# Optimization experiments

Hardware: AMD Instinct MI355X
Metric: run time of the kernel (lower is better)

The kernel has to match this reference:

```python
import jax, jax.numpy as jnp
import numpy as np

D = 2048      # feature dim (fc1 = Linear(2*2048, 2048))
S = 10240


def setup_inputs() -> dict:
    key = jax.random.key(0)
    ks = jax.random.split(key, 16)
    sc = 0.02
    z = lambda *s: jnp.zeros(s, jnp.float32)
    return {
        "x0": jax.random.normal(ks[0], (1, 1, D), jnp.float32),
        "x1": jax.random.normal(ks[1], (1, S, D), jnp.float32),
        # fc1: Linear(4096, 2048)  (stored input-major for x @ W)
        "W1": jax.random.normal(ks[2], (2 * D, D), jnp.float32) * sc,
        "b1": z(D),
        # fc2: Linear(2048, 1)
        "W2": jax.random.normal(ks[3], (D, 1), jnp.float32) * sc,
        "b2": z(1),
        # LSTM(input=1, hidden=1, bidirectional): per-direction gate params [4] = (i,f,g,o)
        "Wih_f": jax.random.normal(ks[4], (4,), jnp.float32) * 0.5,
        "Whh_f": jax.random.normal(ks[5], (4,), jnp.float32) * 0.5,
        "bih_f": z(4),
        "bhh_f": z(4),
        "Wih_b": jax.random.normal(ks[6], (4,), jnp.float32) * 0.5,
        "Whh_b": jax.random.normal(ks[7], (4,), jnp.float32) * 0.5,
        "bih_b": z(4),
        "bhh_b": z(4),
        # fc3: Linear(10, 1)
        "W3": jax.random.normal(ks[8], (10, 1), jnp.float32) * sc,
        "b3": z(1),
    }


def _lstm_dir(x_seq, Wih, Whh, bih, bhh):
    """Single-direction LSTM, input_size=hidden_size=1, batch=1.
    x_seq: [S] scalars. Returns h sequence [S]. PyTorch gate order (i,f,g,o)."""
    b = bih + bhh

    def step(carry, x):
        h, c = carry
        g = Wih * x + Whh * h + b              # [4]
        i = jax.nn.sigmoid(g[0])
        f = jax.nn.sigmoid(g[1])
        gg = jnp.tanh(g[2])
        o = jax.nn.sigmoid(g[3])
        c = f * c + i * gg
        h = o * jnp.tanh(c)
        return (h, c), h

    h0 = jnp.zeros((), x_seq.dtype)
    c0 = jnp.zeros((), x_seq.dtype)
    _, hs = jax.lax.scan(step, (h0, c0), x_seq)
    return hs


def reference(x0, x1, W1, b1, W2, b2,
              Wih_f, Whh_f, bih_f, bhh_f,
              Wih_b, Whh_b, bih_b, bhh_b,
              W3, b3):
    # similarity: cat(|x0 - x1|, x0 + x1) along features (x0 broadcasts over S)
    sim = jnp.concatenate([jnp.abs(x0 - x1), x0 + x1], axis=2)   # [1, S, 2D]
    h = jax.nn.relu(jnp.einsum('bsf,fd->bsd', sim, W1) + b1)     # [1, S, D]
    # (dropout is identity in eval mode)
    s = jax.nn.sigmoid(jnp.einsum('bsd,do->bso', h, W2) + b2)    # [1, S, 1]
    x_seq = s[0, :, 0]                                           # [S]

    h_f = _lstm_dir(x_seq, Wih_f, Whh_f, bih_f, bhh_f)           # [S]
    h_b = _lstm_dir(x_seq[::-1], Wih_b, Whh_b, bih_b, bhh_b)[::-1]
    out = jnp.stack([h_f, h_b], axis=1)                          # [S, 2] == lstm out [S,1,2]

    grp = out.reshape(1, -1, 10)                                 # [1, S*2/10, 10]
    y = jax.nn.sigmoid(grp @ W3 + b3)                            # [1, S*2/10, 1]
    return y.reshape(1, -1)
```

## Files before the change

kernel.cpp:

```cpp
#include <hip/hip_runtime.h>
#include <hip/hip_bf16.h>

#define DD 2048
#define SS 10240
#define KK 4096

typedef __bf16 bf16x8 __attribute__((ext_vector_type(8)));
typedef float  f32x4  __attribute__((ext_vector_type(4)));

__device__ __forceinline__ unsigned short f2bf_rne(float x) {
    unsigned int u = __float_as_uint(x);
    u += 0x7FFFu + ((u >> 16) & 1u);
    return (unsigned short)(u >> 16);
}

__global__ __launch_bounds__(256) void prep_kernel(
    const float* __restrict__ W1, const float* __restrict__ b2,
    unsigned short* __restrict__ W1T, float* __restrict__ s_pre) {
    __shared__ float tile[64][65];
    const int t = threadIdx.x;
    const int bf = blockIdx.x % (KK / 64);
    const int bd = blockIdx.x / (KK / 64);
    const int f0 = bf * 64, d0 = bd * 64;

#pragma unroll
    for (int p = 0; p < 4; ++p) {
        int fr = p * 16 + (t >> 4);
        int dc = (t & 15) * 4;
        const float4 v = *(const float4*)&W1[(size_t)(f0 + fr) * DD + d0 + dc];
        tile[fr][dc + 0] = v.x; tile[fr][dc + 1] = v.y;
        tile[fr][dc + 2] = v.z; tile[fr][dc + 3] = v.w;
    }
    __syncthreads();
#pragma unroll
    for (int p = 0; p < 4; ++p) {
        int dr = p * 16 + (t >> 4);
        int fc = (t & 15) * 4;
        ushort4 o;
        o.x = f2bf_rne(tile[fc + 0][dr]);
        o.y = f2bf_rne(tile[fc + 1][dr]);
        o.z = f2bf_rne(tile[fc + 2][dr]);
        o.w = f2bf_rne(tile[fc + 3][dr]);
        *(ushort4*)&W1T[(size_t)(d0 + dr) * KK + f0 + fc] = o;
    }
    int gid = blockIdx.x * 256 + t;
    if (gid < SS) s_pre[gid] = b2[0];
}

__global__ __launch_bounds__(256) void sim_kernel(
    const float* __restrict__ x0, const float* __restrict__ x1,
    unsigned short* __restrict__ simB) {
    const int s = blockIdx.x;
    const int d = threadIdx.x * 8;
    const float4 a0 = *(const float4*)&x0[d];
    const float4 a1 = *(const float4*)&x0[d + 4];
    const float4 v0 = *(const float4*)&x1[(size_t)s * DD + d];
    const float4 v1 = *(const float4*)&x1[(size_t)s * DD + d + 4];
    ushort4 lo0, lo1, hi0, hi1;
    lo0.x = f2bf_rne(fabsf(a0.x - v0.x)); hi0.x = f2bf_rne(a0.x + v0.x);
    lo0.y = f2bf_rne(fabsf(a0.y - v0.y)); hi0.y = f2bf_rne(a0.y + v0.y);
    lo0.z = f2bf_rne(fabsf(a0.z - v0.z)); hi0.z = f2bf_rne(a0.z + v0.z);
    lo0.w = f2bf_rne(fabsf(a0.w - v0.w)); hi0.w = f2bf_rne(a0.w + v0.w);
    lo1.x = f2bf_rne(fabsf(a1.x - v1.x)); hi1.x = f2bf_rne(a1.x + v1.x);
    lo1.y = f2bf_rne(fabsf(a1.y - v1.y)); hi1.y = f2bf_rne(a1.y + v1.y);
    lo1.z = f2bf_rne(fabsf(a1.z - v1.z)); hi1.z = f2bf_rne(a1.z + v1.z);
    lo1.w = f2bf_rne(fabsf(a1.w - v1.w)); hi1.w = f2bf_rne(a1.w + v1.w);
    unsigned short* row = &simB[(size_t)s * KK];
    *(ushort4*)&row[d]          = lo0;
    *(ushort4*)&row[d + 4]      = lo1;
    *(ushort4*)&row[DD + d]     = hi0;
    *(ushort4*)&row[DD + d + 4] = hi1;
}

#define BM3 320
#define BN3 256
#define BK3 64
#define NKT (KK / BK3)

#define STAGE_A(ktv, BUFV)                                                     \
    _Pragma("unroll")                                                          \
    for (int L = 0; L < 5; ++L) {                                              \
        __builtin_amdgcn_global_load_lds(                                      \
            (const __attribute__((address_space(1))) void*)(gA + (size_t)L * 64 * KK + (size_t)(ktv) * 64), \
            (__attribute__((address_space(3))) void*)&lds[BUFV][t * 8 + L * 4096], \
            16, 0, 0);                                                         \
    }
#define STAGE_B(ktv, BUFV)                                                     \
    _Pragma("unroll")                                                          \
    for (int L = 0; L < 4; ++L) {                                              \
        __builtin_amdgcn_global_load_lds(                                      \
            (const __attribute__((address_space(1))) void*)(gB + (size_t)L * 64 * KK + (size_t)(ktv) * 64), \
            (__attribute__((address_space(3))) void*)&lds[BUFV][20480 + t * 8 + L * 4096], \
            16, 0, 0);                                                         \
    }

#define BODY(ktv, BUF, SA_LIT, SB_LIT, DO_STAGE)                               \
    {                                                                          \
        asm volatile("s_waitcnt vmcnt(" SA_LIT ")" ::: "memory");              \
        __builtin_amdgcn_s_barrier();                                          \
        __builtin_amdgcn_sched_barrier(0);                                     \
        if (DO_STAGE) { STAGE_A((ktv) + 1, BUF ^ 1) }                          \
        asm volatile("s_waitcnt vmcnt(" SB_LIT ")" ::: "memory");              \
        __builtin_amdgcn_s_barrier();                                          \
        __builtin_amdgcn_sched_barrier(0);                                     \
        if (DO_STAGE) { STAGE_B((ktv) + 1, BUF ^ 1) }                          \
        _Pragma("unroll")                                                      \
        for (int ks = 0; ks < 2; ++ks) {                                       \
            const int gx = ks ? gx1 : gx0;                                     \
            _Pragma("unroll")                                                  \
            for (int h = 0; h < 2; ++h) {                                      \
                bf16x8 bfr[4];                                                 \
                _Pragma("unroll")                                              \
                for (int n = 0; n < 4; ++n)                                    \
                    bfr[n] = *(const bf16x8*)&lds[BUF][boff + (h * 4 + n) * 1024 + gx]; \
                _Pragma("unroll")                                              \
                for (int m = 0; m < 5; ++m) {                                  \
                    bf16x8 afr = *(const bf16x8*)&lds[BUF][aoff + m * 1024 + gx]; \
                    __builtin_amdgcn_s_setprio(1);                             \
                    _Pragma("unroll")                                          \
                    for (int n = 0; n < 4; ++n)                                \
                        acc[m][h * 4 + n] = __builtin_amdgcn_mfma_f32_16x16x32_bf16( \
                            afr, bfr[n], acc[m][h * 4 + n], 0, 0, 0);          \
                    __builtin_amdgcn_s_setprio(0);                             \
                }                                                              \
            }                                                                  \
        }                                                                      \
    }

__global__ __launch_bounds__(512, 2) void gemm3_kernel(
    const unsigned short* __restrict__ simB,
    const unsigned short* __restrict__ W1T,
    const float* __restrict__ b1, const float* __restrict__ W2,
    float* __restrict__ s_pre) {
    __shared__ unsigned short lds[2][36864];

    const int t    = threadIdx.x;
    const int lane = t & 63;
    const int wv   = t >> 6;
    const int wr   = wv >> 1;
    const int wc   = wv & 1;
    const int lr   = lane & 15;
    const int g4   = lane >> 4;
    const int l7   = lane & 7;

    const int bn = blockIdx.x & 7;
    const int bm = blockIdx.x >> 3;
    const int m0 = bm * BM3, n0 = bn * BN3;

    const int trow = t >> 3;
    const int gsrc = (t & 7) ^ (trow & 7);
    const unsigned short* gA = simB + (size_t)(m0 + trow) * KK + gsrc * 8;
    const unsigned short* gB = W1T  + (size_t)(n0 + trow) * KK + gsrc * 8;

    const int aoff = (wr * 80 + lr) * 64;
    const int boff = 20480 + (wc * 128 + lr) * 64;
    const int gx0  = ((0 * 4 + g4) ^ l7) * 8;
    const int gx1  = ((1 * 4 + g4) ^ l7) * 8;

    f32x4 acc[5][8];
#pragma unroll
    for (int m = 0; m < 5; ++m)
#pragma unroll
        for (int n = 0; n < 8; ++n)
            acc[m][n] = (f32x4){0.f, 0.f, 0.f, 0.f};

    STAGE_A(0, 0)
    STAGE_B(0, 0)

#pragma unroll 1
    for (int kt = 0; kt < NKT - 2; kt += 2) {
        BODY(kt,     0, "4", "5", 1)
        BODY(kt + 1, 1, "4", "5", 1)
    }
    BODY(NKT - 2, 0, "4", "5", 1)
    BODY(NKT - 1, 1, "4", "0", 0)

    float b1v[8], w2v[8];
#pragma unroll
    for (int n = 0; n < 8; ++n) {
        int col = n0 + wc * 128 + n * 16 + lr;
        b1v[n] = b1[col];
        w2v[n] = W2[col];
    }
#pragma unroll
    for (int m = 0; m < 5; ++m) {
#pragma unroll
        for (int r = 0; r < 4; ++r) {
            float rowsum = 0.f;
#pragma unroll
            for (int n = 0; n < 8; ++n) {
                float v = acc[m][n][r] + b1v[n];
                v = fmaxf(v, 0.f);
                rowsum = fmaf(v, w2v[n], rowsum);
            }
            rowsum += __shfl_xor(rowsum, 1);
            rowsum += __shfl_xor(rowsum, 2);
            rowsum += __shfl_xor(rowsum, 4);
            rowsum += __shfl_xor(rowsum, 8);
            if (lr == 0) {
                int row = m0 + wr * 80 + m * 16 + g4 * 4 + r;
                atomicAdd(&s_pre[row], rowsum);
            }
        }
    }
}

#define BM 128
#define BN 128
#define BK 32

__global__ __launch_bounds__(256) void gemm_kernel(
    const float* __restrict__ x0, const float* __restrict__ x1,
    const unsigned short* __restrict__ W1T,
    const float* __restrict__ b1, const float* __restrict__ W2,
    float* __restrict__ s_pre) {
    __shared__ unsigned short As[BM][BK];
    __shared__ unsigned short Bs[BN][BK];

    const int tid  = threadIdx.x;
    const int lane = tid & 63;
    const int wave = tid >> 6;
    const int wr = wave >> 1, wc = wave & 1;
    const int bm = blockIdx.x / (DD / BN);
    const int bn = blockIdx.x % (DD / BN);
    const int m0 = bm * BM, n0 = bn * BN;
    const int lr = lane & 15;
    const int lk = (lane >> 4) * 8;

    f32x4 acc[4][4];
#pragma unroll
    for (int m = 0; m < 4; ++m)
#pragma unroll
        for (int n = 0; n < 4; ++n)
            acc[m][n] = (f32x4){0.f, 0.f, 0.f, 0.f};

    for (int k0 = 0; k0 < KK; k0 += BK) {
        __syncthreads();
#pragma unroll
        for (int p = 0; p < 2; ++p) {
            int L  = tid + p * 256;
            int n  = L >> 2;
            int k8 = (L & 3) * 8;
            const unsigned short* g = &W1T[(size_t)(n0 + n) * KK + k0 + k8];
            unsigned short* l = &Bs[0][0] + (size_t)L * 8;
            __builtin_amdgcn_global_load_lds(
                (const __attribute__((address_space(1))) void*)g,
                (__attribute__((address_space(3))) void*)l, 16, 0, 0);
        }
        {
            const int f0 = k0 & (DD - 1);
            const bool second = (k0 >= DD);
            const int fc = (tid & 7) * 4;
            const float4 v0 = *(const float4*)&x0[f0 + fc];
#pragma unroll
            for (int p = 0; p < 4; ++p) {
                int row = p * 32 + (tid >> 3);
                const float4 v1 = *(const float4*)&x1[(size_t)(m0 + row) * DD + f0 + fc];
                ushort4 o;
                o.x = f2bf_rne(second ? (v0.x + v1.x) : fabsf(v0.x - v1.x));
                o.y = f2bf_rne(second ? (v0.y + v1.y) : fabsf(v0.y - v1.y));
                o.z = f2bf_rne(second ? (v0.z + v1.z) : fabsf(v0.z - v1.z));
                o.w = f2bf_rne(second ? (v0.w + v1.w) : fabsf(v0.w - v1.w));
                *(ushort4*)&As[row][fc] = o;
            }
        }
        __syncthreads();

        bf16x8 a[4], b[4];
#pragma unroll
        for (int m = 0; m < 4; ++m)
            a[m] = *(const bf16x8*)&As[wr * 64 + m * 16 + lr][lk];
#pragma unroll
        for (int n = 0; n < 4; ++n)
            b[n] = *(const bf16x8*)&Bs[wc * 64 + n * 16 + lr][lk];
#pragma unroll
        for (int m = 0; m < 4; ++m)
#pragma unroll
            for (int n = 0; n < 4; ++n)
                acc[m][n] = __builtin_amdgcn_mfma_f32_16x16x32_bf16(
                    a[m], b[n], acc[m][n], 0, 0, 0);
    }

    float b1v[4], w2v[4];
#pragma unroll
    for (int n = 0; n < 4; ++n) {
        int col = n0 + wc * 64 + n * 16 + lr;
        b1v[n] = b1[col];
        w2v[n] = W2[col];
    }
#pragma unroll
    for (int m = 0; m < 4; ++m) {
#pragma unroll
        for (int r = 0; r < 4; ++r) {
            float rowsum = 0.f;
#pragma unroll
            for (int n = 0; n < 4; ++n) {
                float v = acc[m][n][r] + b1v[n];
                v = fmaxf(v, 0.f);
                rowsum = fmaf(v, w2v[n], rowsum);
            }
            rowsum += __shfl_xor(rowsum, 1);
            rowsum += __shfl_xor(rowsum, 2);
            rowsum += __shfl_xor(rowsum, 4);
            rowsum += __shfl_xor(rowsum, 8);
            if (lr == 0) {
                int row = m0 + wr * 64 + m * 16 + (lane >> 4) * 4 + r;
                atomicAdd(&s_pre[row], rowsum);
            }
        }
    }
}

#define CHUNK 64
#define WARM  192
#define NCH   (SS / CHUNK)

__device__ __forceinline__ float sigf(float x) {
    return 1.f / (1.f + __expf(-x));
}
__device__ __forceinline__ float tanhfast(float x) {
    return 2.f / (1.f + __expf(-2.f * x)) - 1.f;
}

__global__ __launch_bounds__(64) void lstm_kernel(
    const float* __restrict__ s_pre,
    const float* __restrict__ Wih_f, const float* __restrict__ Whh_f,
    const float* __restrict__ bih_f, const float* __restrict__ bhh_f,
    const float* __restrict__ Wih_b, const float* __restrict__ Whh_b,
    const float* __restrict__ bih_b, const float* __restrict__ bhh_b,
    float* __restrict__ hf, float* __restrict__ hb) {
    int id = blockIdx.x * blockDim.x + threadIdx.x;
    if (id >= 2 * NCH) return;
    int dir = id / NCH;
    int ch  = id % NCH;
    const float* Wih = dir ? Wih_b : Wih_f;
    const float* Whh = dir ? Whh_b : Whh_f;
    const float* bih = dir ? bih_b : bih_f;
    const float* bhh = dir ? bhh_b : bhh_f;
    const float wi0 = Wih[0], wi1 = Wih[1], wi2 = Wih[2], wi3 = Wih[3];
    const float wh0 = Whh[0], wh1 = Whh[1], wh2 = Whh[2], wh3 = Whh[3];
    const float bb0 = bih[0] + bhh[0], bb1 = bih[1] + bhh[1];
    const float bb2 = bih[2] + bhh[2], bb3 = bih[3] + bhh[3];

    const int pout0 = ch * CHUNK;
    int pstart = pout0 - WARM; if (pstart < 0) pstart = 0;
    const int pend = pout0 + CHUNK;

    float h = 0.f, c = 0.f;
    for (int p = pstart; p < pend; ++p) {
        int s = dir ? (SS - 1 - p) : p;
        float x  = sigf(s_pre[s]);
        float g0 = fmaf(wi0, x, fmaf(wh0, h, bb0));
        float g1 = fmaf(wi1, x, fmaf(wh1, h, bb1));
        float g2 = fmaf(wi2, x, fmaf(wh2, h, bb2));
        float g3 = fmaf(wi3, x, fmaf(wh3, h, bb3));
        float gi = sigf(g0);
        float gf = sigf(g1);
        float gg = tanhfast(g2);
        float go = sigf(g3);
        c = fmaf(gf, c, gi * gg);
        h = go * tanhfast(c);
        if (p >= pout0) {
            if (dir) hb[s] = h; else hf[s] = h;
        }
    }
}

__global__ __launch_bounds__(256) void final_kernel(
    const float* __restrict__ hf, const float* __restrict__ hb,
    const float* __restrict__ W3, const float* __restrict__ b3,
    float* __restrict__ out) {
    int j = blockIdx.x * blockDim.x + threadIdx.x;
    if (j >= (SS * 2) / 10) return;
    float acc = b3[0];
#pragma unroll
    for (int i = 0; i < 5; ++i) {
        acc = fmaf(hf[5 * j + i], W3[2 * i],     acc);
        acc = fmaf(hb[5 * j + i], W3[2 * i + 1], acc);
    }
    out[j] = sigf(acc);
}

extern "C" void kernel_launch(void* const* d_in, const int* in_sizes, int n_in,
                              void* d_out, int out_size, void* d_ws, size_t ws_size,
                              hipStream_t stream) {
    const float* x0    = (const float*)d_in[0];
    const float* x1    = (const float*)d_in[1];
    const float* W1    = (const float*)d_in[2];
    const float* b1    = (const float*)d_in[3];
    const float* W2    = (const float*)d_in[4];
    const float* b2    = (const float*)d_in[5];
    const float* Wih_f = (const float*)d_in[6];
    const float* Whh_f = (const float*)d_in[7];
    const float* bih_f = (const float*)d_in[8];
    const float* bhh_f = (const float*)d_in[9];
    const float* Wih_b = (const float*)d_in[10];
    const float* Whh_b = (const float*)d_in[11];
    const float* bih_b = (const float*)d_in[12];
    const float* bhh_b = (const float*)d_in[13];
    const float* W3    = (const float*)d_in[14];
    const float* b3    = (const float*)d_in[15];
    float* out = (float*)d_out;

    char* ws = (char*)d_ws;
    const size_t w1t_bytes = (size_t)KK * DD * 2;
    unsigned short* W1T = (unsigned short*)ws;
    float* s_pre = (float*)(ws + w1t_bytes);
    float* hf    = s_pre + SS;
    float* hb    = hf + SS;
    size_t off_sim = w1t_bytes + 3 * (size_t)SS * 4;
    off_sim = (off_sim + 255) & ~(size_t)255;
    unsigned short* simB = (unsigned short*)(ws + off_sim);
    const size_t need = off_sim + (size_t)SS * KK * 2;

    prep_kernel<<<(KK / 64) * (DD / 64), 256, 0, stream>>>(W1, b2, W1T, s_pre);
    if (ws_size >= need) {
        sim_kernel<<<SS, 256, 0, stream>>>(x0, x1, simB);
        gemm3_kernel<<<(SS / BM3) * (DD / BN3), 512, 0, stream>>>(
            simB, W1T, b1, W2, s_pre);
    } else {
        gemm_kernel<<<(SS / BM) * (DD / BN), 256, 0, stream>>>(
            x0, x1, W1T, b1, W2, s_pre);
    }
    lstm_kernel<<<(2 * NCH + 63) / 64, 64, 0, stream>>>(
        s_pre, Wih_f, Whh_f, bih_f, bhh_f, Wih_b, Whh_b, bih_b, bhh_b, hf, hb);
    final_kernel<<<((SS * 2) / 10 + 255) / 256, 256, 0, stream>>>(hf, hb, W3, b3, out);
}
```

Baseline: 415.9 us.

## Merge prep and sim kernels, load all B fragments at once, reorder block mapping

Folds the W1 transpose/convert kernel and the similarity-building kernel into one launch by giving each role its own block index range, which removes one launch and the serialization between them. Inside the GEMM main loop, all eight B fragments are loaded from LDS up front instead of in two halves, so each A fragment feeds eight MFMAs. This raises register pressure under a 2-blocks-per-CU launch bound. The block-to-tile mapping also changes so consecutive blocks walk down M for a fixed N column, which alters L2 reuse of the W1T and simB tiles.

```diff
diff --git a/kernel.cpp b/kernel.cpp
--- a/kernel.cpp
+++ b/kernel.cpp
@@ -14,62 +14,62 @@
     return (unsigned short)(u >> 16);
 }
 
-__global__ __launch_bounds__(256) void prep_kernel(
+__global__ __launch_bounds__(256) void prep_sim_kernel(
     const float* __restrict__ W1, const float* __restrict__ b2,
-    unsigned short* __restrict__ W1T, float* __restrict__ s_pre) {
+    const float* __restrict__ x0, const float* __restrict__ x1,
+    unsigned short* __restrict__ W1T, float* __restrict__ s_pre,
+    unsigned short* __restrict__ simB) {
     __shared__ float tile[64][65];
     const int t = threadIdx.x;
-    const int bf = blockIdx.x % (KK / 64);
-    const int bd = blockIdx.x / (KK / 64);
-    const int f0 = bf * 64, d0 = bd * 64;
-
-#pragma unroll
-    for (int p = 0; p < 4; ++p) {
-        int fr = p * 16 + (t >> 4);
-        int dc = (t & 15) * 4;
-        const float4 v = *(const float4*)&W1[(size_t)(f0 + fr) * DD + d0 + dc];
-        tile[fr][dc + 0] = v.x; tile[fr][dc + 1] = v.y;
-        tile[fr][dc + 2] = v.z; tile[fr][dc + 3] = v.w;
-    }
-    __syncthreads();
-#pragma unroll
-    for (int p = 0; p < 4; ++p) {
-        int dr = p * 16 + (t >> 4);
-        int fc = (t & 15) * 4;
-        ushort4 o;
-        o.x = f2bf_rne(tile[fc + 0][dr]);
-        o.y = f2bf_rne(tile[fc + 1][dr]);
-        o.z = f2bf_rne(tile[fc + 2][dr]);
-        o.w = f2bf_rne(tile[fc + 3][dr]);
-        *(ushort4*)&W1T[(size_t)(d0 + dr) * KK + f0 + fc] = o;
-    }
-    int gid = blockIdx.x * 256 + t;
-    if (gid < SS) s_pre[gid] = b2[0];
-}
-
-__global__ __launch_bounds__(256) void sim_kernel(
-    const float* __restrict__ x0, const float* __restrict__ x1,
-    unsigned short* __restrict__ simB) {
-    const int s = blockIdx.x;
-    const int d = threadIdx.x * 8;
-    const float4 a0 = *(const float4*)&x0[d];
-    const float4 a1 = *(const float4*)&x0[d + 4];
-    const float4 v0 = *(const float4*)&x1[(size_t)s * DD + d];
-    const float4 v1 = *(const float4*)&x1[(size_t)s * DD + d + 4];
-    ushort4 lo0, lo1, hi0, hi1;
-    lo0.x = f2bf_rne(fabsf(a0.x - v0.x)); hi0.x = f2bf_rne(a0.x + v0.x);
-    lo0.y = f2bf_rne(fabsf(a0.y - v0.y)); hi0.y = f2bf_rne(a0.y + v0.y);
-    lo0.z = f2bf_rne(fabsf(a0.z - v0.z)); hi0.z = f2bf_rne(a0.z + v0.z);
-    lo0.w = f2bf_rne(fabsf(a0.w - v0.w)); hi0.w = f2bf_rne(a0.w + v0.w);
-    lo1.x = f2bf_rne(fabsf(a1.x - v1.x)); hi1.x = f2bf_rne(a1.x + v1.x);
-    lo1.y = f2bf_rne(fabsf(a1.y - v1.y)); hi1.y = f2bf_rne(a1.y + v1.y);
-    lo1.z = f2bf_rne(fabsf(a1.z - v1.z)); hi1.z = f2bf_rne(a1.z + v1.z);
-    lo1.w = f2bf_rne(fabsf(a1.w - v1.w)); hi1.w = f2bf_rne(a1.w + v1.w);
-    unsigned short* row = &simB[(size_t)s * KK];
-    *(ushort4*)&row[d]          = lo0;
-    *(ushort4*)&row[d + 4]      = lo1;
-    *(ushort4*)&row[DD + d]     = hi0;
-    *(ushort4*)&row[DD + d + 4] = hi1;
+
+    if (blockIdx.x < (KK / 64) * (DD / 64)) {
+        const int bf = blockIdx.x % (KK / 64);
+        const int bd = blockIdx.x / (KK / 64);
+        const int f0 = bf * 64, d0 = bd * 64;
+#pragma unroll
+        for (int p = 0; p < 4; ++p) {
+            int fr = p * 16 + (t >> 4);
+            int dc = (t & 15) * 4;
+            const float4 v = *(const float4*)&W1[(size_t)(f0 + fr) * DD + d0 + dc];
+            tile[fr][dc + 0] = v.x; tile[fr][dc + 1] = v.y;
+            tile[fr][dc + 2] = v.z; tile[fr][dc + 3] = v.w;
+        }
+        __syncthreads();
+#pragma unroll
+        for (int p = 0; p < 4; ++p) {
+            int dr = p * 16 + (t >> 4);
+            int fc = (t & 15) * 4;
+            ushort4 o;
+            o.x = f2bf_rne(tile[fc + 0][dr]);
+            o.y = f2bf_rne(tile[fc + 1][dr]);
+            o.z = f2bf_rne(tile[fc + 2][dr]);
+            o.w = f2bf_rne(tile[fc + 3][dr]);
+            *(ushort4*)&W1T[(size_t)(d0 + dr) * KK + f0 + fc] = o;
+        }
+        int gid = blockIdx.x * 256 + t;
+        if (gid < SS) s_pre[gid] = b2[0];
+    } else {
+        const int s = blockIdx.x - (KK / 64) * (DD / 64);
+        const int d = t * 8;
+        const float4 a0 = *(const float4*)&x0[d];
+        const float4 a1 = *(const float4*)&x0[d + 4];
+        const float4 v0 = *(const float4*)&x1[(size_t)s * DD + d];
+        const float4 v1 = *(const float4*)&x1[(size_t)s * DD + d + 4];
+        ushort4 lo0, lo1, hi0, hi1;
+        lo0.x = f2bf_rne(fabsf(a0.x - v0.x)); hi0.x = f2bf_rne(a0.x + v0.x);
+        lo0.y = f2bf_rne(fabsf(a0.y - v0.y)); hi0.y = f2bf_rne(a0.y + v0.y);
+        lo0.z = f2bf_rne(fabsf(a0.z - v0.z)); hi0.z = f2bf_rne(a0.z + v0.z);
+        lo0.w = f2bf_rne(fabsf(a0.w - v0.w)); hi0.w = f2bf_rne(a0.w + v0.w);
+        lo1.x = f2bf_rne(fabsf(a1.x - v1.x)); hi1.x = f2bf_rne(a1.x + v1.x);
+        lo1.y = f2bf_rne(fabsf(a1.y - v1.y)); hi1.y = f2bf_rne(a1.y + v1.y);
+        lo1.z = f2bf_rne(fabsf(a1.z - v1.z)); hi1.z = f2bf_rne(a1.z + v1.z);
+        lo1.w = f2bf_rne(fabsf(a1.w - v1.w)); hi1.w = f2bf_rne(a1.w + v1.w);
+        unsigned short* row = &simB[(size_t)s * KK];
+        *(ushort4*)&row[d]          = lo0;
+        *(ushort4*)&row[d + 4]      = lo1;
+        *(ushort4*)&row[DD + d]     = hi0;
+        *(ushort4*)&row[DD + d + 4] = hi1;
+    }
 }
 
 #define BM3 320
@@ -107,22 +107,19 @@
         _Pragma("unroll")                                                      \
         for (int ks = 0; ks < 2; ++ks) {                                       \
             const int gx = ks ? gx1 : gx0;                                     \
+            bf16x8 bfr[8];                                                     \
             _Pragma("unroll")                                                  \
-            for (int h = 0; h < 2; ++h) {                                      \
-                bf16x8 bfr[4];                                                 \
+            for (int n = 0; n < 8; ++n)                                        \
+                bfr[n] = *(const bf16x8*)&lds[BUF][boff + n * 1024 + gx];      \
+            _Pragma("unroll")                                                  \
+            for (int m = 0; m < 5; ++m) {                                      \
+                bf16x8 afr = *(const bf16x8*)&lds[BUF][aoff + m * 1024 + gx];  \
+                __builtin_amdgcn_s_setprio(1);                                 \
                 _Pragma("unroll")                                              \
-                for (int n = 0; n < 4; ++n)                                    \
-                    bfr[n] = *(const bf16x8*)&lds[BUF][boff + (h * 4 + n) * 1024 + gx]; \
-                _Pragma("unroll")                                              \
-                for (int m = 0; m < 5; ++m) {                                  \
-                    bf16x8 afr = *(const bf16x8*)&lds[BUF][aoff + m * 1024 + gx]; \
-                    __builtin_amdgcn_s_setprio(1);                             \
-                    _Pragma("unroll")                                          \
-                    for (int n = 0; n < 4; ++n)                                \
-                        acc[m][h * 4 + n] = __builtin_amdgcn_mfma_f32_16x16x32_bf16( \
-                            afr, bfr[n], acc[m][h * 4 + n], 0, 0, 0);          \
-                    __builtin_amdgcn_s_setprio(0);                             \
-                }                                                              \
+                for (int n = 0; n < 8; ++n)                                    \
+                    acc[m][n] = __builtin_amdgcn_mfma_f32_16x16x32_bf16(       \
+                        afr, bfr[n], acc[m][n], 0, 0, 0);                      \
+                __builtin_amdgcn_s_setprio(0);                                 \
             }                                                                  \
         }                                                                      \
     }
@@ -143,8 +140,8 @@
     const int g4   = lane >> 4;
     const int l7   = lane & 7;
 
-    const int bn = blockIdx.x & 7;
-    const int bm = blockIdx.x >> 3;
+    const int bm = blockIdx.x & 31;
+    const int bn = blockIdx.x >> 5;
     const int m0 = bm * BM3, n0 = bn * BN3;
 
     const int trow = t >> 3;
@@ -413,12 +410,14 @@
     unsigned short* simB = (unsigned short*)(ws + off_sim);
     const size_t need = off_sim + (size_t)SS * KK * 2;
 
-    prep_kernel<<<(KK / 64) * (DD / 64), 256, 0, stream>>>(W1, b2, W1T, s_pre);
     if (ws_size >= need) {
-        sim_kernel<<<SS, 256, 0, stream>>>(x0, x1, simB);
+        prep_sim_kernel<<<(KK / 64) * (DD / 64) + SS, 256, 0, stream>>>(
+            W1, b2, x0, x1, W1T, s_pre, simB);
         gemm3_kernel<<<(SS / BM3) * (DD / BN3), 512, 0, stream>>>(
             simB, W1T, b1, W2, s_pre);
     } else {
+        prep_sim_kernel<<<(KK / 64) * (DD / 64), 256, 0, stream>>>(
+            W1, b2, x0, x1, W1T, s_pre, simB);
         gemm_kernel<<<(SS / BM) * (DD / BN), 256, 0, stream>>>(
             x0, x1, W1T, b1, W2, s_pre);
     }
```

Result: faster. 400.3 us (-3.7%).
